# Performance work log

Hardware: AMD Instinct MI355X
Metric: run time of the kernel (lower is better)

## Reference

```python
import jax, jax.numpy as jnp
import numpy as np

B, T, C = 1, 4096, 1024
H = 16
D = C // H  # 64
LN_EPS = 1e-5


def layer_norm(x, g, b):
    mu = jnp.mean(x, axis=-1, keepdims=True)
    var = jnp.mean(jnp.square(x - mu), axis=-1, keepdims=True)
    return (x - mu) * jax.lax.rsqrt(var + LN_EPS) * g + b


def setup_inputs() -> dict:
    key = jax.random.key(0)
    ks = jax.random.split(key, 8)
    s = 0.02
    return {
        "x": jax.random.normal(ks[0], (B, T, C), dtype=jnp.float32),
        "ln1_g": jnp.ones((C,), jnp.float32),
        "ln1_b": jnp.zeros((C,), jnp.float32),
        "Wqkv": jax.random.normal(ks[1], (C, 3 * C), dtype=jnp.float32) * s,
        "bqkv": jnp.zeros((3 * C,), jnp.float32),
        "Wo": jax.random.normal(ks[2], (C, C), dtype=jnp.float32) * s,
        "bo": jnp.zeros((C,), jnp.float32),
        "ln2_g": jnp.ones((C,), jnp.float32),
        "ln2_b": jnp.zeros((C,), jnp.float32),
        "W1": jax.random.normal(ks[3], (C, 4 * C), dtype=jnp.float32) * s,
        "b1": jnp.zeros((4 * C,), jnp.float32),
        "W2": jax.random.normal(ks[4], (4 * C, C), dtype=jnp.float32) * s,
        "b2": jnp.zeros((C,), jnp.float32),
    }


def reference(x, ln1_g, ln1_b, Wqkv, bqkv, Wo, bo, ln2_g, ln2_b, W1, b1, W2, b2):
    b, t, c = x.shape
    x_norm = layer_norm(x, ln1_g, ln1_b)
    qkv = x_norm @ Wqkv + bqkv                      # [B,T,3C]
    qkv = qkv.reshape(b, t, 3, H, D).transpose(2, 0, 3, 1, 4)  # [3,B,H,T,D]
    Q, K, V = qkv[0], qkv[1], qkv[2]
    scores = jnp.einsum("bhtd,bhsd->bhts", Q, K) / jnp.sqrt(jnp.float32(D))
    causal = jnp.tril(jnp.ones((t, t), dtype=bool))  # [T,T]
    scores = jnp.where(causal[None, None], scores, -jnp.inf)
    weights = jax.nn.softmax(scores, axis=-1)
    attn = jnp.einsum("bhts,bhsd->bhtd", weights, V)  # [B,H,T,D]
    attn = attn.transpose(0, 2, 1, 3).reshape(b, t, c)
    x = x + (attn @ Wo + bo)
    h = layer_norm(x, ln2_g, ln2_b)
    h = jax.nn.gelu(h @ W1 + b1, approximate=False) @ W2 + b2
    return x + h
```

## Files before the change

### kernel.cpp

```cpp
#include <hip/hip_runtime.h>
#include <math.h>

typedef __bf16 bf16_t;
typedef __attribute__((ext_vector_type(8))) __bf16 bf16x8;
typedef __attribute__((ext_vector_type(4))) __bf16 bf16x4;
typedef __attribute__((ext_vector_type(4))) float f32x4;
typedef __attribute__((ext_vector_type(16))) float f32x16;
typedef __attribute__((ext_vector_type(4))) unsigned int u32x4;

#define T_LEN 4096
#define C_DIM 1024
#define NH 16
#define HD 64

__device__ __forceinline__ void gload_lds16(const void* g, void* l) {
    __builtin_amdgcn_global_load_lds(
        (__attribute__((address_space(1))) void*)(g),
        (__attribute__((address_space(3))) void*)(l), 16, 0, 0);
}

__device__ __forceinline__ f32x4 mfma16(bf16x8 a, bf16x8 b, f32x4 c) {
    return __builtin_amdgcn_mfma_f32_16x16x32_bf16(a, b, c, 0, 0, 0);
}

__device__ __forceinline__ f32x16 mfma32(bf16x8 a, bf16x8 b, f32x16 c) {
    return __builtin_amdgcn_mfma_f32_32x32x16_bf16(a, b, c, 0, 0, 0);
}

__device__ __forceinline__ float gelu_exact(float v) {
    return 0.5f * v * (1.0f + erff(v * 0.7071067811865476f));
}

__device__ __forceinline__ void make_frags2(const f32x16 s, bf16x8& fx, bf16x8& fy) {
    unsigned a0, a1, b0, b1;
    asm("v_cvt_pk_bf16_f32 %0, %1, %2" : "=v"(a0) : "v"(s[0]), "v"(s[1]));
    asm("v_cvt_pk_bf16_f32 %0, %1, %2" : "=v"(a1) : "v"(s[2]), "v"(s[3]));
    asm("v_cvt_pk_bf16_f32 %0, %1, %2" : "=v"(b0) : "v"(s[4]), "v"(s[5]));
    asm("v_cvt_pk_bf16_f32 %0, %1, %2" : "=v"(b1) : "v"(s[6]), "v"(s[7]));
    asm("v_permlane32_swap_b32 %0, %1" : "+v"(a0), "+v"(b0));
    asm("v_permlane32_swap_b32 %0, %1" : "+v"(a1), "+v"(b1));
    u32x4 wa = {a0, a1, b0, b1};
    fx = __builtin_bit_cast(bf16x8, wa);
    unsigned c0, c1, d0, d1;
    asm("v_cvt_pk_bf16_f32 %0, %1, %2" : "=v"(c0) : "v"(s[8]), "v"(s[9]));
    asm("v_cvt_pk_bf16_f32 %0, %1, %2" : "=v"(c1) : "v"(s[10]), "v"(s[11]));
    asm("v_cvt_pk_bf16_f32 %0, %1, %2" : "=v"(d0) : "v"(s[12]), "v"(s[13]));
    asm("v_cvt_pk_bf16_f32 %0, %1, %2" : "=v"(d1) : "v"(s[14]), "v"(s[15]));
    asm("v_permlane32_swap_b32 %0, %1" : "+v"(c0), "+v"(d0));
    asm("v_permlane32_swap_b32 %0, %1" : "+v"(c1), "+v"(d1));
    u32x4 wb = {c0, c1, d0, d1};
    fy = __builtin_bit_cast(bf16x8, wb);
}

__global__ __launch_bounds__(256) void transpose_all(
    const float* __restrict__ wqkv, const float* __restrict__ wo,
    const float* __restrict__ w1, const float* __restrict__ w2,
    bf16_t* __restrict__ oqkv, bf16_t* __restrict__ owo,
    bf16_t* __restrict__ ow1, bf16_t* __restrict__ ow2)
{
    __shared__ float tile[32][33];
    int s = blockIdx.x;
    const float* in; bf16_t* out; int R, C, NBX;
    if (s < 3072)      {            in = wqkv; out = oqkv; R = 1024; C = 3072; NBX = 96; }
    else if (s < 4096) { s -= 3072; in = wo;   out = owo;  R = 1024; C = 1024; NBX = 32; }
    else if (s < 8192) { s -= 4096; in = w1;   out = ow1;  R = 1024; C = 4096; NBX = 128; }
    else               { s -= 8192; in = w2;   out = ow2;  R = 4096; C = 1024; NBX = 32; }
    const int tx = threadIdx.x, ty = threadIdx.y;
    const int c0 = (s % NBX) * 32, r0 = (s / NBX) * 32;
#pragma unroll
    for (int j = 0; j < 4; ++j)
        tile[ty + j * 8][tx] = in[(size_t)(r0 + ty + j * 8) * C + c0 + tx];
    __syncthreads();
#pragma unroll
    for (int j = 0; j < 4; ++j)
        out[(size_t)(c0 + ty + j * 8) * R + r0 + tx] = (bf16_t)tile[tx][ty + j * 8];
}

__global__ __launch_bounds__(256) void ln_bf16(
    const float* __restrict__ x, const float* __restrict__ gam,
    const float* __restrict__ bet, bf16_t* __restrict__ out)
{
    const int row = blockIdx.x, t = threadIdx.x;
    const float4 v = *(const float4*)(x + (size_t)row * 1024 + t * 4);
    float s1 = v.x + v.y + v.z + v.w;
    float s2 = v.x * v.x + v.y * v.y + v.z * v.z + v.w * v.w;
#pragma unroll
    for (int m = 1; m < 64; m <<= 1) {
        s1 += __shfl_xor(s1, m);
        s2 += __shfl_xor(s2, m);
    }
    __shared__ float red[8];
    if ((t & 63) == 0) { red[(t >> 6) * 2] = s1; red[(t >> 6) * 2 + 1] = s2; }
    __syncthreads();
    s1 = red[0] + red[2] + red[4] + red[6];
    s2 = red[1] + red[3] + red[5] + red[7];
    const float mu = s1 * (1.0f / 1024.0f);
    const float inv = rsqrtf(s2 * (1.0f / 1024.0f) - mu * mu + 1e-5f);
    const float4 gg = *(const float4*)(gam + t * 4);
    const float4 bb = *(const float4*)(bet + t * 4);
    bf16x4 o;
    o[0] = (bf16_t)((v.x - mu) * inv * gg.x + bb.x);
    o[1] = (bf16_t)((v.y - mu) * inv * gg.y + bb.y);
    o[2] = (bf16_t)((v.z - mu) * inv * gg.z + bb.z);
    o[3] = (bf16_t)((v.w - mu) * inv * gg.w + bb.w);
    *(bf16x4*)(out + (size_t)row * 1024 + t * 4) = o;
}

template <int EPI>
__global__ __launch_bounds__(256, 2) void gemm_bt(
    const bf16_t* __restrict__ A, const bf16_t* __restrict__ Bt,
    const float* __restrict__ bias, const float* __restrict__ res,
    bf16_t* __restrict__ outb, float* __restrict__ outf,
    int M, int N, int Klen, int Kstr)
{
    __shared__ alignas(1024) bf16_t Alds[4][128 * 32];
    __shared__ alignas(1024) bf16_t Blds[4][128 * 32];
    const int t = threadIdx.x;
    const int lane = t & 63, w = t >> 6;
    const int wr = w >> 1, wc = w & 1;
    const int g = lane >> 4, ci = lane & 15;

    int bx, by, chunk = 0;
    if constexpr (EPI == 3) {
        const int flat = blockIdx.x + 8 * blockIdx.y;
        const int xcd = flat & 7, s = flat >> 3;
        chunk = s >> 5;
        const int s2 = s & 31;
        by = xcd * 4 + (s2 >> 3);
        bx = s2 & 7;
        A  += (size_t)chunk * Klen;
        Bt += (size_t)chunk * Klen;
    } else {
        const int NB = gridDim.x, MB = gridDim.y;
        const int flat = blockIdx.x + NB * blockIdx.y;
        const int xcd = flat & 7, slot = flat >> 3;
        by = xcd * (MB >> 3) + slot / NB;
        bx = slot % NB;
    }
    const int m0 = by * 128, n0 = bx * 128;

    f32x4 acc[4][4];
#pragma unroll
    for (int i = 0; i < 4; ++i)
#pragma unroll
        for (int j = 0; j < 4; ++j)
#pragma unroll
            for (int k = 0; k < 4; ++k) acc[i][j][k] = 0.0f;

    const int r0 = t >> 2;
    const int cc = (t & 3) * 8;
    const int nkt = Klen >> 5;

    auto stage = [&](int kt) {
        const int b = kt & 3;
        const int kk = kt * 32;
        char* aB = (char*)&Alds[b][0] + w * 1024;
        char* bB = (char*)&Blds[b][0] + w * 1024;
        gload_lds16(A + (size_t)(m0 + r0) * Kstr + kk + cc, aB);
        gload_lds16(A + (size_t)(m0 + r0 + 64) * Kstr + kk + cc, aB + 4096);
        gload_lds16(Bt + (size_t)(n0 + r0) * Kstr + kk + cc, bB);
        gload_lds16(Bt + (size_t)(n0 + r0 + 64) * Kstr + kk + cc, bB + 4096);
    };

    stage(0);
    if (nkt > 1) stage(1);
    for (int kt = 0; kt < nkt; ++kt) {
        if (kt + 2 < nkt) {
            stage(kt + 2);
            asm volatile("s_waitcnt vmcnt(8)" ::: "memory");
        } else if (kt + 1 < nkt) {
            asm volatile("s_waitcnt vmcnt(4)" ::: "memory");
        } else {
            asm volatile("s_waitcnt vmcnt(0)" ::: "memory");
        }
        __builtin_amdgcn_s_barrier();
        __builtin_amdgcn_sched_barrier(0);
        const int b = kt & 3;
        const bf16_t* ap = &Alds[b][0] + (wr * 64 + ci) * 32 + g * 8;
        const bf16_t* bp = &Blds[b][0] + (wc * 64 + ci) * 32 + g * 8;
        bf16x8 af[4], bf[4];
#pragma unroll
        for (int mt = 0; mt < 4; ++mt) af[mt] = *(const bf16x8*)(ap + mt * 16 * 32);
#pragma unroll
        for (int nt = 0; nt < 4; ++nt) bf[nt] = *(const bf16x8*)(bp + nt * 16 * 32);
        __builtin_amdgcn_s_setprio(1);
#pragma unroll
        for (int mt = 0; mt < 4; ++mt)
#pragma unroll
            for (int nt = 0; nt < 4; ++nt)
                acc[mt][nt] = mfma16(af[mt], bf[nt], acc[mt][nt]);
        __builtin_amdgcn_s_setprio(0);
    }

#pragma unroll
    for (int nt = 0; nt < 4; ++nt) {
        const int col = n0 + wc * 64 + nt * 16 + ci;
        const float bv = (EPI == 3) ? 0.0f : bias[col];
#pragma unroll
        for (int mt = 0; mt < 4; ++mt) {
            const int row = m0 + wr * 64 + mt * 16 + g * 4;
#pragma unroll
            for (int r = 0; r < 4; ++r) {
                float v = acc[mt][nt][r] + bv;
                if constexpr (EPI == 1) v = gelu_exact(v);
                if constexpr (EPI == 2) {
                    outf[(size_t)(row + r) * N + col] =
                        v + res[(size_t)(row + r) * N + col];
                } else if constexpr (EPI == 3) {
                    outf[((size_t)chunk * M + row + r) * N + col] = v;
                } else {
                    outb[(size_t)(row + r) * N + col] = (bf16_t)v;
                }
            }
        }
    }
}

__global__ __launch_bounds__(256) void w2_combine(
    const float* __restrict__ part, const float* __restrict__ bias,
    const float* __restrict__ res, float* __restrict__ out)
{
    const int row = blockIdx.x, t = threadIdx.x;
    const int c = t * 4;
    const float4 a = *(const float4*)(part + (size_t)row * 1024 + c);
    const float4 b = *(const float4*)(part + ((size_t)T_LEN + row) * 1024 + c);
    const float4 rr = *(const float4*)(res + (size_t)row * 1024 + c);
    const float4 bb = *(const float4*)(bias + c);
    float4 o;
    o.x = a.x + b.x + rr.x + bb.x;
    o.y = a.y + b.y + rr.y + bb.y;
    o.z = a.z + b.z + rr.z + bb.z;
    o.w = a.w + b.w + rr.w + bb.w;
    *(float4*)(out + (size_t)row * 1024 + c) = o;
}

template <int EPI>
__global__ __launch_bounds__(512, 2) void gemm256(
    const bf16_t* __restrict__ A, const bf16_t* __restrict__ Bt,
    const float* __restrict__ bias, bf16_t* __restrict__ outb,
    bf16_t* __restrict__ vtout, int M, int N, int K)
{
    __shared__ alignas(1024) bf16_t lds[2][2][256 * 64];
    const int t = threadIdx.x, lane = t & 63, w = t >> 6;
    const int g = lane >> 4, ci = lane & 15;
    const int wr = w >> 2, wc = w & 3;
    const int NB = gridDim.x;
    const int nwg = NB * gridDim.y;
    const int flat = blockIdx.x + NB * blockIdx.y;
    const int rix = (flat & 7) * (nwg >> 3) + (flat >> 3);
    const int m0 = (rix / NB) * 256, n0 = (rix % NB) * 256;
    const int NKT = K >> 6;

    f32x4 acc[8][4];
#pragma unroll
    for (int i = 0; i < 8; ++i)
#pragma unroll
        for (int j = 0; j < 4; ++j)
#pragma unroll
            for (int k2 = 0; k2 < 4; ++k2) acc[i][j][k2] = 0.0f;

    const int sw0 = (g ^ (ci & 7)) * 8;
    const int sw1 = ((4 + g) ^ (ci & 7)) * 8;

    auto stage = [&](int h, int ktile, int b) {
#pragma unroll
        for (int i = 0; i < 2; ++i) {
            const int idx = i * 512 + t;
            const int r = idx >> 3;
            const int c = (t & 7) ^ (r & 7);
            const bf16_t* src = ((h < 2) ? A : Bt)
                + (size_t)(((h < 2) ? m0 : n0) + (h & 1) * 128 + r) * K
                + ktile * 64 + c * 8;
            bf16_t* dst = &lds[b][h >> 1][(h & 1) * 8192] + (i * 512 + w * 64) * 8;
            gload_lds16(src, dst);
        }
    };

    bf16x8 a[4][2], b2[2][2][2];

    stage(0, 0, 0); stage(3, 0, 0); stage(1, 0, 0); stage(2, 0, 0);
    if (NKT > 1) { stage(0, 1, 1); stage(3, 1, 1); stage(1, 1, 1); }
    asm volatile("s_waitcnt vmcnt(6)" ::: "memory");
    __builtin_amdgcn_s_barrier();

    for (int kt = 0; kt < NKT; ++kt) {
        const int cur = kt & 1;
        const bf16_t* Ab = &lds[cur][0][0];
        const bf16_t* Bb = &lds[cur][1][0];

#pragma unroll
        for (int mi = 0; mi < 4; ++mi) {
            const bf16_t* ap = Ab + (wr * 64 + mi * 16 + ci) * 64;
            a[mi][0] = *(const bf16x8*)(ap + sw0);
            a[mi][1] = *(const bf16x8*)(ap + sw1);
        }
#pragma unroll
        for (int ni = 0; ni < 2; ++ni) {
            const bf16_t* bp = Bb + (wc * 32 + ni * 16 + ci) * 64;
            b2[0][ni][0] = *(const bf16x8*)(bp + sw0);
            b2[0][ni][1] = *(const bf16x8*)(bp + sw1);
        }
        if (kt + 1 < NKT) stage(2, kt + 1, cur ^ 1);
        __builtin_amdgcn_s_barrier();
        asm volatile("s_waitcnt lgkmcnt(0)" ::: "memory");
        __builtin_amdgcn_sched_barrier(0);
        __builtin_amdgcn_s_setprio(1);
#pragma unroll
        for (int mi = 0; mi < 4; ++mi)
#pragma unroll
            for (int ni = 0; ni < 2; ++ni) {
                acc[mi][ni] = mfma16(a[mi][0], b2[0][ni][0], acc[mi][ni]);
                acc[mi][ni] = mfma16(a[mi][1], b2[0][ni][1], acc[mi][ni]);
            }
        __builtin_amdgcn_s_setprio(0);
        __builtin_amdgcn_s_barrier();

#pragma unroll
        for (int ni = 0; ni < 2; ++ni) {
            const bf16_t* bp = Bb + (128 + wc * 32 + ni * 16 + ci) * 64;
            b2[1][ni][0] = *(const bf16x8*)(bp + sw0);
            b2[1][ni][1] = *(const bf16x8*)(bp + sw1);
        }
        if (kt + 2 < NKT) stage(0, kt + 2, cur);
        __builtin_amdgcn_s_barrier();
        asm volatile("s_waitcnt lgkmcnt(0)" ::: "memory");
        __builtin_amdgcn_sched_barrier(0);
        __builtin_amdgcn_s_setprio(1);
#pragma unroll
        for (int mi = 0; mi < 4; ++mi)
#pragma unroll
            for (int ni = 0; ni < 2; ++ni) {
                acc[mi][2 + ni] = mfma16(a[mi][0], b2[1][ni][0], acc[mi][2 + ni]);
                acc[mi][2 + ni] = mfma16(a[mi][1], b2[1][ni][1], acc[mi][2 + ni]);
            }
        __builtin_amdgcn_s_setprio(0);
        __builtin_amdgcn_s_barrier();

#pragma unroll
        for (int mi = 0; mi < 4; ++mi) {
            const bf16_t* ap = Ab + (128 + wr * 64 + mi * 16 + ci) * 64;
            a[mi][0] = *(const bf16x8*)(ap + sw0);
            a[mi][1] = *(const bf16x8*)(ap + sw1);
        }
        if (kt + 2 < NKT) stage(3, kt + 2, cur);
        __builtin_amdgcn_s_barrier();
        asm volatile("s_waitcnt lgkmcnt(0)" ::: "memory");
        __builtin_amdgcn_sched_barrier(0);
        __builtin_amdgcn_s_setprio(1);
#pragma unroll
        for (int mi = 0; mi < 4; ++mi)
#pragma unroll
            for (int ni = 0; ni < 2; ++ni) {
                acc[4 + mi][2 + ni] = mfma16(a[mi][0], b2[1][ni][0], acc[4 + mi][2 + ni]);
                acc[4 + mi][2 + ni] = mfma16(a[mi][1], b2[1][ni][1], acc[4 + mi][2 + ni]);
            }
        __builtin_amdgcn_s_setprio(0);
        __builtin_amdgcn_s_barrier();

        if (kt + 2 < NKT) stage(1, kt + 2, cur);
        __builtin_amdgcn_s_barrier();
        __builtin_amdgcn_s_setprio(1);
#pragma unroll
        for (int mi = 0; mi < 4; ++mi)
#pragma unroll
            for (int ni = 0; ni < 2; ++ni) {
                acc[4 + mi][ni] = mfma16(a[mi][0], b2[0][ni][0], acc[4 + mi][ni]);
                acc[4 + mi][ni] = mfma16(a[mi][1], b2[0][ni][1], acc[4 + mi][ni]);
            }
        __builtin_amdgcn_s_setprio(0);
        if (kt + 2 < NKT) asm volatile("s_waitcnt vmcnt(6)" ::: "memory");
        else              asm volatile("s_waitcnt vmcnt(0)" ::: "memory");
        __builtin_amdgcn_s_barrier();
    }

    const float QSC = 0.125f * 1.4426950408889634f;
#pragma unroll
    for (int mrep = 0; mrep < 8; ++mrep) {
        const int row = m0 + (mrep >> 2) * 128 + wr * 64 + (mrep & 3) * 16 + g * 4;
#pragma unroll
        for (int nrep = 0; nrep < 4; ++nrep) {
            const int col = n0 + (nrep >> 1) * 128 + wc * 32 + (nrep & 1) * 16 + ci;
            const float bv = bias[col];
            if (EPI == 2 && col >= 2048) {
                const int cv = col - 2048;
                bf16x4 o4;
#pragma unroll
                for (int jr = 0; jr < 4; ++jr)
                    o4[jr] = (bf16_t)(acc[mrep][nrep][jr] + bv);
                *(bf16x4*)(vtout + (size_t)(cv >> 6) * 262144
                           + (size_t)(cv & 63) * 4096 + row) = o4;
            } else {
                const float sc = (EPI == 2 && col < 1024) ? QSC : 1.0f;
#pragma unroll
                for (int jr = 0; jr < 4; ++jr) {
                    float v = acc[mrep][nrep][jr] + bv;
                    if constexpr (EPI == 1) v = gelu_exact(v);
                    if (EPI == 2) v *= sc;
                    outb[(size_t)(row + jr) * N + col] = (bf16_t)v;
                }
            }
        }
    }
}

__global__ __launch_bounds__(256, 2) void attn_fwd(
    const bf16_t* __restrict__ qkv, const bf16_t* __restrict__ vt,
    bf16_t* __restrict__ opart, float* __restrict__ lbuf)
{
    __shared__ alignas(1024) bf16_t Klds[2][64 * 64];
    __shared__ alignas(1024) bf16_t Vlds[2][64 * 64];
    const int t = threadIdx.x, lane = t & 63, w = t >> 6;
    const int hi = lane >> 5, li = lane & 31;
    const int lq = li >> 2;
    const int h = blockIdx.x;
    const int y = blockIdx.y;
    const int qt = 31 - (y >> 1);
    const int chunk = y & 1;
    const int q0 = qt * 128;
    const int qrow = q0 + w * 32 + li;
    const int wDiag = 2 * qt + (w >> 1);
    const int ktA = chunk ? (qt + 1) : 0;
    const int ktB = chunk ? (2 * qt + 2) : (qt + 1);

    bf16x8 qf[4];
#pragma unroll
    for (int ks = 0; ks < 4; ++ks)
        qf[ks] = *(const bf16x8*)(qkv + (size_t)qrow * 3072 + h * 64 + ks * 16 + hi * 8);
    bf16x8 ones8;
#pragma unroll
    for (int j = 0; j < 8; ++j) ones8[j] = (bf16_t)1.0f;

    f32x16 oacc[2], lacc;
#pragma unroll
    for (int r = 0; r < 16; ++r) { oacc[0][r] = 0.0f; oacc[1][r] = 0.0f; lacc[r] = 0.0f; }

    const int sr = t >> 3;
    const int sx = ((t & 7) ^ ((sr >> 2) & 7)) * 8;

    auto stageKV = [&](int kt, int b) {
        const size_t kbase = (size_t)(kt * 64) * 3072 + 1024 + h * 64 + sx;
        const size_t vbase = (size_t)h * 262144 + (size_t)kt * 64 + sx;
#pragma unroll
        for (int i = 0; i < 2; ++i) {
            gload_lds16(qkv + kbase + (size_t)(i * 32 + sr) * 3072,
                        (char*)&Klds[b][0] + (size_t)(i * 2048 + t * 8) * 2);
            gload_lds16(vt + vbase + (size_t)(i * 32 + sr) * 4096,
                        (char*)&Vlds[b][0] + (size_t)(i * 2048 + t * 8) * 2);
        }
    };

    stageKV(ktA, 0);
    for (int kt = ktA; kt < ktB; ++kt) {
        const int cur = (kt - ktA) & 1;
        asm volatile("s_waitcnt vmcnt(0)" ::: "memory");
        __syncthreads();
        if (kt + 1 < ktB) stageKV(kt + 1, cur ^ 1);

        if (kt <= wDiag) {
            const bf16_t* Kb = &Klds[cur][0];
            const bf16_t* Vb = &Vlds[cur][0];
            f32x16 s0, s1;
#pragma unroll
            for (int r = 0; r < 16; ++r) { s0[r] = 0.0f; s1[r] = 0.0f; }

            __builtin_amdgcn_s_setprio(1);
#pragma unroll
            for (int ks = 0; ks < 4; ++ks) {
                const int cs = ((ks * 2 + hi) ^ lq) * 8;
                s0 = mfma32(*(const bf16x8*)(Kb + li * 64 + cs), qf[ks], s0);
                s1 = mfma32(*(const bf16x8*)(Kb + (32 + li) * 64 + cs), qf[ks], s1);
            }
            __builtin_amdgcn_s_setprio(0);

            bf16x8 vf[4][2];
#pragma unroll
            for (int ks = 0; ks < 4; ++ks) {
                const int cs = ((ks * 2 + hi) ^ lq) * 8;
                vf[ks][0] = *(const bf16x8*)(Vb + li * 64 + cs);
                vf[ks][1] = *(const bf16x8*)(Vb + (32 + li) * 64 + cs);
            }

            if (kt == wDiag) {
                const int kb0 = kt * 64 + 4 * hi;
#pragma unroll
                for (int r = 0; r < 16; ++r) {
                    const int kp0 = kb0 + (r & 3) + 8 * (r >> 2);
                    if (kp0 > qrow) s0[r] = -1e30f;
                    if (kp0 + 32 > qrow) s1[r] = -1e30f;
                }
            }
#pragma unroll
            for (int r = 0; r < 16; ++r) {
                s0[r] = exp2f(s0[r]);
                s1[r] = exp2f(s1[r]);
            }

            bf16x8 pf[4];
            make_frags2(s0, pf[0], pf[1]);
            make_frags2(s1, pf[2], pf[3]);

            __builtin_amdgcn_s_setprio(1);
#pragma unroll
            for (int ks = 0; ks < 4; ++ks) {
                oacc[0] = mfma32(vf[ks][0], pf[ks], oacc[0]);
                oacc[1] = mfma32(vf[ks][1], pf[ks], oacc[1]);
                lacc    = mfma32(ones8,     pf[ks], lacc);
            }
            __builtin_amdgcn_s_setprio(0);
        }
        __syncthreads();
    }

    bf16_t* op = opart + ((size_t)chunk * T_LEN + qrow) * 1024 + h * 64 + hi * 4;
#pragma unroll
    for (int dblk = 0; dblk < 2; ++dblk)
#pragma unroll
        for (int gi = 0; gi < 4; ++gi) {
            bf16x4 o4;
#pragma unroll
            for (int j = 0; j < 4; ++j) o4[j] = (bf16_t)oacc[dblk][gi * 4 + j];
            *(bf16x4*)(op + dblk * 32 + gi * 8) = o4;
        }
    if (hi == 0)
        lbuf[((size_t)chunk * T_LEN + qrow) * NH + h] = lacc[0];
}

__global__ __launch_bounds__(256) void attn_combine(
    const bf16_t* __restrict__ opart, const float* __restrict__ lbuf,
    bf16_t* __restrict__ out)
{
    const int row = blockIdx.x, t = threadIdx.x;
    const int c = t * 4, h = c >> 6;
    const float l0 = lbuf[(size_t)row * NH + h];
    const float l1 = lbuf[((size_t)T_LEN + row) * NH + h];
    const float inv = 1.0f / (l0 + l1);
    const bf16x4 o0 = *(const bf16x4*)(opart + (size_t)row * 1024 + c);
    const bf16x4 o1 = *(const bf16x4*)(opart + ((size_t)T_LEN + row) * 1024 + c);
    bf16x4 o;
#pragma unroll
    for (int j = 0; j < 4; ++j)
        o[j] = (bf16_t)(((float)o0[j] + (float)o1[j]) * inv);
    *(bf16x4*)(out + (size_t)row * 1024 + c) = o;
}

extern "C" void kernel_launch(void* const* d_in, const int* in_sizes, int n_in,
                              void* d_out, int out_size, void* d_ws, size_t ws_size,
                              hipStream_t stream)
{
    const float* x    = (const float*)d_in[0];
    const float* ln1g = (const float*)d_in[1];
    const float* ln1b = (const float*)d_in[2];
    const float* Wqkv = (const float*)d_in[3];
    const float* bqkv = (const float*)d_in[4];
    const float* Wo   = (const float*)d_in[5];
    const float* bo   = (const float*)d_in[6];
    const float* ln2g = (const float*)d_in[7];
    const float* ln2b = (const float*)d_in[8];
    const float* W1   = (const float*)d_in[9];
    const float* b1   = (const float*)d_in[10];
    const float* W2   = (const float*)d_in[11];
    const float* b2   = (const float*)d_in[12];
    float* outp = (float*)d_out;

    char* p = (char*)d_ws;
    bf16_t* WqkvT = (bf16_t*)p; p += (size_t)3072 * 1024 * 2;
    bf16_t* WoT   = (bf16_t*)p; p += (size_t)1024 * 1024 * 2;
    bf16_t* W1T   = (bf16_t*)p; p += (size_t)4096 * 1024 * 2;
    bf16_t* W2T   = (bf16_t*)p; p += (size_t)1024 * 4096 * 2;
    bf16_t* xn    = (bf16_t*)p; p += (size_t)4096 * 1024 * 2;
    bf16_t* qkv   = (bf16_t*)p; p += (size_t)4096 * 3072 * 2;
    bf16_t* vtb   = (bf16_t*)p; p += (size_t)16 * 64 * 4096 * 2;
    bf16_t* attnb = (bf16_t*)p; p += (size_t)4096 * 1024 * 2;
    float*  x2    = (float*)p;  p += (size_t)4096 * 1024 * 4;
    bf16_t* hb    = (bf16_t*)p; p += (size_t)4096 * 1024 * 2;
    bf16_t* g1    = (bf16_t*)p; p += (size_t)4096 * 4096 * 2;
    bf16_t* opart = (bf16_t*)p; p += (size_t)2 * 4096 * 1024 * 2;
    float*  lbuf  = (float*)p;  p += (size_t)2 * 4096 * 16 * 4;
    float*  w2part = (float*)p; p += (size_t)2 * 4096 * 1024 * 4;

    transpose_all<<<12288, dim3(32, 8), 0, stream>>>(Wqkv, Wo, W1, W2,
                                                     WqkvT, WoT, W1T, W2T);

    ln_bf16<<<4096, 256, 0, stream>>>(x, ln1g, ln1b, xn);
    gemm256<2><<<dim3(12, 16), 512, 0, stream>>>(xn, WqkvT, bqkv,
                                                 qkv, vtb, 4096, 3072, 1024);
    attn_fwd<<<dim3(16, 64), 256, 0, stream>>>(qkv, vtb, opart, lbuf);
    attn_combine<<<4096, 256, 0, stream>>>(opart, lbuf, attnb);
    gemm_bt<2><<<dim3(8, 32), 256, 0, stream>>>(attnb, WoT, bo, x,
                                                nullptr, x2, 4096, 1024, 1024, 1024);
    ln_bf16<<<4096, 256, 0, stream>>>(x2, ln2g, ln2b, hb);
    gemm256<1><<<dim3(16, 16), 512, 0, stream>>>(hb, W1T, b1,
                                                 g1, nullptr, 4096, 4096, 1024);
    gemm_bt<3><<<dim3(8, 64), 256, 0, stream>>>(g1, W2T, nullptr, nullptr,
                                                nullptr, w2part, 4096, 1024, 2048, 4096);
    w2_combine<<<4096, 256, 0, stream>>>(w2part, b2, x2, outp);
}
```

Before: 257.8 us.

## Fuse W2 split-K halves into one 512-thread block with LDS reduction

Replaces the two-chunk split-K W2 GEMM plus separate combine kernel with a single kernel. Each 512-thread block runs two 256-thread groups, one per K half, and reduces their partials through LDS before adding bias and residual in the epilogue. This drops the fp32 partial buffer round trip to global memory and one kernel launch. In exchange, occupancy falls to one block per CU with 128 KB of LDS, and the grid shrinks from 512 to 256 blocks.

```diff
diff --git a/kernel.cpp b/kernel.cpp
--- a/kernel.cpp
+++ b/kernel.cpp
@@ -120,23 +120,11 @@
     const int wr = w >> 1, wc = w & 1;
     const int g = lane >> 4, ci = lane & 15;
 
-    int bx, by, chunk = 0;
-    if constexpr (EPI == 3) {
-        const int flat = blockIdx.x + 8 * blockIdx.y;
-        const int xcd = flat & 7, s = flat >> 3;
-        chunk = s >> 5;
-        const int s2 = s & 31;
-        by = xcd * 4 + (s2 >> 3);
-        bx = s2 & 7;
-        A  += (size_t)chunk * Klen;
-        Bt += (size_t)chunk * Klen;
-    } else {
-        const int NB = gridDim.x, MB = gridDim.y;
-        const int flat = blockIdx.x + NB * blockIdx.y;
-        const int xcd = flat & 7, slot = flat >> 3;
-        by = xcd * (MB >> 3) + slot / NB;
-        bx = slot % NB;
-    }
+    const int NB = gridDim.x, MB = gridDim.y;
+    const int flat = blockIdx.x + NB * blockIdx.y;
+    const int xcd = flat & 7, slot = flat >> 3;
+    const int by = xcd * (MB >> 3) + slot / NB;
+    const int bx = slot % NB;
     const int m0 = by * 128, n0 = bx * 128;
 
     f32x4 acc[4][4];
@@ -195,7 +183,7 @@
 #pragma unroll
     for (int nt = 0; nt < 4; ++nt) {
         const int col = n0 + wc * 64 + nt * 16 + ci;
-        const float bv = (EPI == 3) ? 0.0f : bias[col];
+        const float bv = bias[col];
 #pragma unroll
         for (int mt = 0; mt < 4; ++mt) {
             const int row = m0 + wr * 64 + mt * 16 + g * 4;
@@ -206,8 +194,6 @@
                 if constexpr (EPI == 2) {
                     outf[(size_t)(row + r) * N + col] =
                         v + res[(size_t)(row + r) * N + col];
-                } else if constexpr (EPI == 3) {
-                    outf[((size_t)chunk * M + row + r) * N + col] = v;
                 } else {
                     outb[(size_t)(row + r) * N + col] = (bf16_t)v;
                 }
@@ -216,22 +202,111 @@
     }
 }
 
-__global__ __launch_bounds__(256) void w2_combine(
-    const float* __restrict__ part, const float* __restrict__ bias,
-    const float* __restrict__ res, float* __restrict__ out)
-{
-    const int row = blockIdx.x, t = threadIdx.x;
-    const int c = t * 4;
-    const float4 a = *(const float4*)(part + (size_t)row * 1024 + c);
-    const float4 b = *(const float4*)(part + ((size_t)T_LEN + row) * 1024 + c);
-    const float4 rr = *(const float4*)(res + (size_t)row * 1024 + c);
-    const float4 bb = *(const float4*)(bias + c);
-    float4 o;
-    o.x = a.x + b.x + rr.x + bb.x;
-    o.y = a.y + b.y + rr.y + bb.y;
-    o.z = a.z + b.z + rr.z + bb.z;
-    o.w = a.w + b.w + rr.w + bb.w;
-    *(float4*)(out + (size_t)row * 1024 + c) = o;
+__global__ __launch_bounds__(512, 1) void gemm_w2(
+    const bf16_t* __restrict__ A, const bf16_t* __restrict__ Bt,
+    const float* __restrict__ bias, const float* __restrict__ res,
+    float* __restrict__ out, int M, int N, int Khalf, int Kstr)
+{
+    __shared__ alignas(1024) char smem[131072];
+    bf16_t* ring = (bf16_t*)smem;
+    const int t = threadIdx.x;
+    const int grp = t >> 8, tl = t & 255;
+    const int lane = tl & 63, w = tl >> 6;
+    const int wr = w >> 1, wc = w & 1;
+    const int g = lane >> 4, ci = lane & 15;
+
+    const int NB = gridDim.x, MB = gridDim.y;
+    const int flat = blockIdx.x + NB * blockIdx.y;
+    const int xcd = flat & 7, slot = flat >> 3;
+    const int by = xcd * (MB >> 3) + slot / NB;
+    const int bx = slot % NB;
+    const int m0 = by * 128, n0 = bx * 128;
+
+    const bf16_t* Ag = A + (size_t)grp * Khalf;
+    const bf16_t* Bg = Bt + (size_t)grp * Khalf;
+
+    f32x4 acc[4][4];
+#pragma unroll
+    for (int i = 0; i < 4; ++i)
+#pragma unroll
+        for (int j = 0; j < 4; ++j)
+#pragma unroll
+            for (int k = 0; k < 4; ++k) acc[i][j][k] = 0.0f;
+
+    const int r0 = tl >> 2;
+    const int cc = (tl & 3) * 8;
+    const int nkt = Khalf >> 5;
+
+    auto stage = [&](int kt) {
+        const int b = kt & 3;
+        const int kk = kt * 32;
+        bf16_t* base = ring + grp * 32768 + b * 8192;
+        char* aB = (char*)base + w * 1024;
+        char* bB = (char*)(base + 4096) + w * 1024;
+        gload_lds16(Ag + (size_t)(m0 + r0) * Kstr + kk + cc, aB);
+        gload_lds16(Ag + (size_t)(m0 + r0 + 64) * Kstr + kk + cc, aB + 4096);
+        gload_lds16(Bg + (size_t)(n0 + r0) * Kstr + kk + cc, bB);
+        gload_lds16(Bg + (size_t)(n0 + r0 + 64) * Kstr + kk + cc, bB + 4096);
+    };
+
+    stage(0);
+    stage(1);
+    for (int kt = 0; kt < nkt; ++kt) {
+        if (kt + 2 < nkt) {
+            stage(kt + 2);
+            asm volatile("s_waitcnt vmcnt(8)" ::: "memory");
+        } else if (kt + 1 < nkt) {
+            asm volatile("s_waitcnt vmcnt(4)" ::: "memory");
+        } else {
+            asm volatile("s_waitcnt vmcnt(0)" ::: "memory");
+        }
+        __builtin_amdgcn_s_barrier();
+        __builtin_amdgcn_sched_barrier(0);
+        const bf16_t* base = ring + grp * 32768 + (kt & 3) * 8192;
+        const bf16_t* ap = base + (wr * 64 + ci) * 32 + g * 8;
+        const bf16_t* bp = base + 4096 + (wc * 64 + ci) * 32 + g * 8;
+        bf16x8 af[4], bf[4];
+#pragma unroll
+        for (int mt = 0; mt < 4; ++mt) af[mt] = *(const bf16x8*)(ap + mt * 16 * 32);
+#pragma unroll
+        for (int nt = 0; nt < 4; ++nt) bf[nt] = *(const bf16x8*)(bp + nt * 16 * 32);
+        __builtin_amdgcn_s_setprio(1);
+#pragma unroll
+        for (int mt = 0; mt < 4; ++mt)
+#pragma unroll
+            for (int nt = 0; nt < 4; ++nt)
+                acc[mt][nt] = mfma16(af[mt], bf[nt], acc[mt][nt]);
+        __builtin_amdgcn_s_setprio(0);
+    }
+
+    __syncthreads();
+    float* ex = (float*)smem;
+    if (grp == 1) {
+#pragma unroll
+        for (int mt = 0; mt < 4; ++mt)
+#pragma unroll
+            for (int nt = 0; nt < 4; ++nt)
+                *(f32x4*)(ex + tl * 68 + (mt * 4 + nt) * 4) = acc[mt][nt];
+    }
+    __syncthreads();
+    if (grp == 0) {
+#pragma unroll
+        for (int nt = 0; nt < 4; ++nt) {
+            const int col = n0 + wc * 64 + nt * 16 + ci;
+            const float bv = bias[col];
+#pragma unroll
+            for (int mt = 0; mt < 4; ++mt) {
+                const int row = m0 + wr * 64 + mt * 16 + g * 4;
+                const f32x4 p1 = *(const f32x4*)(ex + tl * 68 + (mt * 4 + nt) * 4);
+#pragma unroll
+                for (int r = 0; r < 4; ++r) {
+                    out[(size_t)(row + r) * N + col] =
+                        acc[mt][nt][r] + p1[r] + bv +
+                        res[(size_t)(row + r) * N + col];
+                }
+            }
+        }
+    }
 }
 
 template <int EPI>
@@ -576,7 +651,6 @@
     bf16_t* g1    = (bf16_t*)p; p += (size_t)4096 * 4096 * 2;
     bf16_t* opart = (bf16_t*)p; p += (size_t)2 * 4096 * 1024 * 2;
     float*  lbuf  = (float*)p;  p += (size_t)2 * 4096 * 16 * 4;
-    float*  w2part = (float*)p; p += (size_t)2 * 4096 * 1024 * 4;
 
     transpose_all<<<12288, dim3(32, 8), 0, stream>>>(Wqkv, Wo, W1, W2,
                                                      WqkvT, WoT, W1T, W2T);
@@ -591,7 +665,6 @@
     ln_bf16<<<4096, 256, 0, stream>>>(x2, ln2g, ln2b, hb);
     gemm256<1><<<dim3(16, 16), 512, 0, stream>>>(hb, W1T, b1,
                                                  g1, nullptr, 4096, 4096, 1024);
-    gemm_bt<3><<<dim3(8, 64), 256, 0, stream>>>(g1, W2T, nullptr, nullptr,
-                                                nullptr, w2part, 4096, 1024, 2048, 4096);
-    w2_combine<<<4096, 256, 0, stream>>>(w2part, b2, x2, outp);
-}
+    gemm_w2<<<dim3(8, 32), 512, 0, stream>>>(g1, W2T, b2, x2,
+                                             outp, 4096, 1024, 2048, 4096);
+}
```

Result: faster. 246.1 us (-4.6%).
